# Performance work log

Measured on AMD Instinct MI355X. Metric: run time of the kernel, lower is better.

Reference implementation:

```python
import jax, jax.numpy as jnp
import numpy as np

E, IN, HID, OUT, B = 8, 512, 512, 512, 1024
BN_EPS = 1e-5

def _init_w(key, e, i, o):
    bound = np.sqrt(6.0 / (i * o))
    return jax.random.uniform(key, (e, i, o), dtype=jnp.float32, minval=-bound, maxval=bound)

def setup_inputs() -> dict:
    key = jax.random.key(0)
    k = jax.random.split(key, 6)
    x = jax.random.normal(k[0], (B, IN), dtype=jnp.float32)
    coef = jax.random.uniform(k[1], (B, E), dtype=jnp.float32)
    coef = coef / jnp.sum(coef, axis=-1, keepdims=True)  # soft blending weights
    w1 = _init_w(k[2], E, IN, HID)
    b1 = jnp.zeros((E, HID), dtype=jnp.float32)
    w2 = _init_w(k[3], E, HID, OUT)
    b2 = jnp.zeros((E, OUT), dtype=jnp.float32)
    gamma = jnp.ones((HID,), dtype=jnp.float32)
    beta = jnp.zeros((HID,), dtype=jnp.float32)
    return {"x": x, "blending_coef": coef, "w1": w1, "b1": b1,
            "w2": w2, "b2": b2, "gamma": gamma, "beta": beta}

def reference(x, blending_coef, w1, b1, w2, b2, gamma, beta):
    # layer 1: per-sample blended linear. Same math as
    # sum(coef[...,None,None]*w1, dim=1) applied via sum(x[...,None]*W, dim=1),
    # expressed as one contraction to avoid the [B,I,H] intermediate.
    h = jnp.einsum('be,eih,bi->bh', blending_coef, w1, x) + blending_coef @ b1
    # BatchNorm1d (training mode: batch stats, biased variance) + affine
    mean = jnp.mean(h, axis=0)
    var = jnp.mean((h - mean) ** 2, axis=0)
    hn = (h - mean) * jax.lax.rsqrt(var + BN_EPS) * gamma + beta
    h1 = jax.nn.elu(hn)
    # layer 2
    out = jnp.einsum('be,eho,bh->bo', blending_coef, w2, h1) + blending_coef @ b2
    return out
```

## Files before the change

kernel.cpp:

```cpp
#include <hip/hip_runtime.h>


typedef short bf16x8 __attribute__((ext_vector_type(8)));
typedef float f32x4 __attribute__((ext_vector_type(4)));
typedef unsigned short u16;
typedef u16 u16x4 __attribute__((ext_vector_type(4)));
typedef u16 u16x8 __attribute__((ext_vector_type(8)));

__device__ __forceinline__ u16 f2bf(float f) {
  union { float f; unsigned u; } v; v.f = f;
  return (u16)((v.u + 0x7FFFu + ((v.u >> 16) & 1u)) >> 16);
}
__device__ __forceinline__ float bf2f(u16 u) {
  union { unsigned u; float f; } v; v.u = (unsigned)u << 16; return v.f;
}

__global__ __launch_bounds__(256) void prep1_kernel(
    const float* __restrict__ x, const float* __restrict__ w1,
    u16* __restrict__ xbp, u16* __restrict__ w1p)
{
  int bid = blockIdx.x, t = threadIdx.x;
  __shared__ float ld[64][65];
  if (bid < 64) {
    int g = bid, ri = t & 15, q = t >> 4;
    #pragma unroll
    for (int rep = 0; rep < 4; ++rep) {
      int chunk = rep * 16 + q;
      int s = chunk >> 2, c = chunk & 3;
      const float* src = x + (size_t)(g * 16 + ri) * 512 + s * 32 + c * 8;
      f32x4 v0 = *(const f32x4*)src;
      f32x4 v1 = *(const f32x4*)(src + 4);
      u16x8 o;
      #pragma unroll
      for (int i = 0; i < 4; ++i) { o[i] = f2bf(v0[i]); o[4 + i] = f2bf(v1[i]); }
      *(u16x8*)(xbp + ((size_t)(g * 16 + s) * 64 + c * 16 + ri) * 8) = o;
    }
    return;
  }
  int job = bid - 64;
  int e = job >> 6, tl = job & 63;
  int kt = tl >> 3, nt = tl & 7;
  #pragma unroll
  for (int j = 0; j < 4; ++j) {
    int kr = j * 16 + (t >> 4), nc = (t & 15) * 4;
    f32x4 v = *(const f32x4*)(w1 + (size_t)(e * 512 + kt * 64 + kr) * 512 + nt * 64 + nc);
    ld[kr][nc] = v.x; ld[kr][nc + 1] = v.y; ld[kr][nc + 2] = v.z; ld[kr][nc + 3] = v.w;
  }
  __syncthreads();
  #pragma unroll
  for (int rep = 0; rep < 2; ++rep) {
    int gidx = rep * 256 + t;
    int ri = gidx & 15, c = (gidx >> 4) & 3, sl = (gidx >> 6) & 1, grp = gidx >> 7;
    int n_local = grp * 16 + ri;
    int gn = nt * 4 + grp, s = kt * 2 + sl, k0 = sl * 32 + c * 8;
    u16x8 o;
    #pragma unroll
    for (int i = 0; i < 8; ++i) o[i] = f2bf(ld[k0 + i][n_local]);
    *(u16x8*)(w1p + ((size_t)((e * 32 + gn) * 16 + s) * 64 + c * 16 + ri) * 8) = o;
  }
}

__global__ __launch_bounds__(512, 2) void gemm1_prep2(
    const u16* __restrict__ Ap, const u16* __restrict__ Wp,
    const float* __restrict__ coef, const float* __restrict__ bias,
    const float* __restrict__ w2, u16* __restrict__ w2p,
    u16* __restrict__ hb, float* __restrict__ sP, float* __restrict__ qP)
{
  __shared__ __align__(16) char smem[38912];
  int t = threadIdx.x;
  if (blockIdx.x >= 256) {
    float (*ld)[65] = (float (*)[65])smem;
    int job = blockIdx.x - 256;
    int e = job >> 6, tl = job & 63;
    int kt = tl >> 3, nt = tl & 7;
    #pragma unroll
    for (int j = 0; j < 2; ++j) {
      int kr = j * 32 + (t >> 4), nc = (t & 15) * 4;
      f32x4 v = *(const f32x4*)(w2 + (size_t)(e * 512 + kt * 64 + kr) * 512 + nt * 64 + nc);
      ld[kr][nc] = v.x; ld[kr][nc + 1] = v.y; ld[kr][nc + 2] = v.z; ld[kr][nc + 3] = v.w;
    }
    __syncthreads();
    {
      int ri = t & 15, c = (t >> 4) & 3, sl = (t >> 6) & 1, grp = t >> 7;
      int n_local = grp * 16 + ri;
      int gn = nt * 4 + grp, s = kt * 2 + sl, k0 = sl * 32 + c * 8;
      u16x8 o;
      #pragma unroll
      for (int i = 0; i < 8; ++i) o[i] = f2bf(ld[k0 + i][n_local]);
      *(u16x8*)(w2p + ((size_t)((e * 32 + gn) * 16 + s) * 64 + c * 16 + ri) * 8) = o;
    }
    return;
  }
  float* red = (float*)smem;
  f32x4* partS = (f32x4*)(smem + 34816);
  f32x4* partQ = (f32x4*)(smem + 34816 + 2048);
  int raw = blockIdx.x, nt = raw & 7, mt = raw >> 3;
  int l = t & 63, e = t >> 6;

  const u16* Ab = Ap + (size_t)(mt * 2) * 16 * 512 + l * 8;
  const u16* Bb = Wp + (size_t)(e * 32 + nt * 4) * 16 * 512 + l * 8;

  f32x4 acc[2][4] = {};
  bf16x8 bfr[3][4], afr[2][2];
  #pragma unroll
  for (int n = 0; n < 4; ++n) {
    bfr[0][n] = *(const bf16x8*)(Bb + (size_t)n * 16 * 512);
    bfr[1][n] = *(const bf16x8*)(Bb + (size_t)n * 16 * 512 + 512);
  }
  #pragma unroll
  for (int m = 0; m < 2; ++m)
    afr[0][m] = *(const bf16x8*)(Ab + (size_t)m * 16 * 512);

  #pragma unroll
  for (int s = 0; s < 16; ++s) {
    const int cb = s % 3, nb = (s + 2) % 3, ca = s & 1, na = ca ^ 1;
    if (s < 14) {
      #pragma unroll
      for (int n = 0; n < 4; ++n)
        bfr[nb][n] = *(const bf16x8*)(Bb + (size_t)n * 16 * 512 + (s + 2) * 512);
    }
    if (s < 15) {
      #pragma unroll
      for (int m = 0; m < 2; ++m)
        afr[na][m] = *(const bf16x8*)(Ab + (size_t)m * 16 * 512 + (s + 1) * 512);
    }
    #pragma unroll
    for (int m = 0; m < 2; ++m)
      #pragma unroll
      for (int n = 0; n < 4; ++n)
        acc[m][n] = __builtin_amdgcn_mfma_f32_16x16x32_bf16(afr[ca][m], bfr[cb][n], acc[m][n], 0, 0, 0);
  }

  int rl = (l >> 4) * 4;
  #pragma unroll
  for (int m = 0; m < 2; ++m)
    #pragma unroll
    for (int r = 0; r < 4; ++r) {
      float cf = coef[(size_t)(mt * 32 + m * 16 + rl + r) * 8 + e];
      #pragma unroll
      for (int n = 0; n < 4; ++n) acc[m][n][r] *= cf;
    }

#define RED_STORE(slot)                                                       \
  { _Pragma("unroll") for (int m = 0; m < 2; ++m)                             \
    _Pragma("unroll") for (int n = 0; n < 4; ++n)                             \
    _Pragma("unroll") for (int r = 0; r < 4; ++r)                             \
      red[(slot) * 2176 + (m * 16 + rl + r) * 68 + n * 16 + (l & 15)] = acc[m][n][r]; }
#define RED_ADD(slot)                                                         \
  { _Pragma("unroll") for (int m = 0; m < 2; ++m)                             \
    _Pragma("unroll") for (int n = 0; n < 4; ++n)                             \
    _Pragma("unroll") for (int r = 0; r < 4; ++r)                             \
      acc[m][n][r] += red[(slot) * 2176 + (m * 16 + rl + r) * 68 + n * 16 + (l & 15)]; }

  if (e >= 4) RED_STORE(e - 4);
  __syncthreads();
  if (e < 4) { RED_ADD(e); RED_STORE(e); }
  __syncthreads();

  {
    int row = t >> 4, c0 = (t & 15) * 4;
    f32x4 v = {0.f, 0.f, 0.f, 0.f};
    #pragma unroll
    for (int sl = 0; sl < 4; ++sl)
      v += *(const f32x4*)&red[sl * 2176 + row * 68 + c0];
    int rowg = mt * 32 + row, colg = nt * 64 + c0;
    f32x4 cv0 = *(const f32x4*)(coef + (size_t)rowg * 8);
    f32x4 cv1 = *(const f32x4*)(coef + (size_t)rowg * 8 + 4);
    #pragma unroll
    for (int e2 = 0; e2 < 4; ++e2) {
      v += cv0[e2] * *(const f32x4*)(bias + e2 * 512 + colg);
      v += cv1[e2] * *(const f32x4*)(bias + (e2 + 4) * 512 + colg);
    }
    f32x4 ss = v, qq = v * v;
    #pragma unroll
    for (int i = 0; i < 4; ++i) {
      ss[i] += __shfl_xor(ss[i], 16); ss[i] += __shfl_xor(ss[i], 32);
      qq[i] += __shfl_xor(qq[i], 16); qq[i] += __shfl_xor(qq[i], 32);
    }
    int w = t >> 6;
    if (l < 16) { partS[w * 16 + l] = ss; partQ[w * 16 + l] = qq; }
    u16x4 o;
    #pragma unroll
    for (int i = 0; i < 4; ++i) o[i] = f2bf(v[i]);
    int g = row >> 4, ri = row & 15;
    int spk = nt * 2 + (c0 >> 5), cpk = (c0 >> 3) & 3, j = c0 & 7;
    *(u16x4*)(hb + ((size_t)((mt * 2 + g) * 16 + spk) * 64 + cpk * 16 + ri) * 8 + j) = o;
  }
  __syncthreads();
  if (t < 16) {
    f32x4 S = {0.f, 0.f, 0.f, 0.f}, Q = {0.f, 0.f, 0.f, 0.f};
    #pragma unroll
    for (int w = 0; w < 8; ++w) { S += partS[w * 16 + t]; Q += partQ[w * 16 + t]; }
    *(f32x4*)(sP + mt * 512 + nt * 64 + t * 4) = S;
    *(f32x4*)(qP + mt * 512 + nt * 64 + t * 4) = Q;
  }
#undef RED_STORE
#undef RED_ADD
}

__global__ __launch_bounds__(512, 2) void gemm2_kernel(
    const u16* __restrict__ hb, const u16* __restrict__ Wp,
    const float* __restrict__ coef, const float* __restrict__ bias,
    const float* __restrict__ gamma, const float* __restrict__ beta,
    const float* __restrict__ sP, const float* __restrict__ qP,
    float* __restrict__ Out)
{
  __shared__ __align__(16) char smem[34816];
  __shared__ float sc[512], sh[512];
  u16* As = (u16*)smem;
  float* red = (float*)smem;
  int raw = blockIdx.x, nt = raw & 7, mt = raw >> 3;
  int t = threadIdx.x, l = t & 63, e = t >> 6;

  const u16* Bb = Wp + (size_t)(e * 32 + nt * 4) * 16 * 512 + l * 8;
  bf16x8 bfr[3][4];
  #pragma unroll
  for (int n = 0; n < 4; ++n) {
    bfr[0][n] = *(const bf16x8*)(Bb + (size_t)n * 16 * 512);
    bfr[1][n] = *(const bf16x8*)(Bb + (size_t)n * 16 * 512 + 512);
  }

  {
    float S = 0.f, Q = 0.f;
    #pragma unroll
    for (int p = 0; p < 32; ++p) { S += sP[p * 512 + t]; Q += qP[p * 512 + t]; }
    float mean = S * (1.0f / 1024.0f);
    float var  = Q * (1.0f / 1024.0f) - mean * mean;
    float s_ = gamma[t] * rsqrtf(var + 1e-5f);
    sc[t] = s_; sh[t] = beta[t] - mean * s_;
  }
  __syncthreads();

  const u16* hsrc = hb + (size_t)mt * 16384;
  #pragma unroll
  for (int rep = 0; rep < 4; ++rep) {
    int ci = rep * 512 + t;
    u16x8 hv = *(const u16x8*)(hsrc + (size_t)ci * 8);
    int s = (ci >> 6) & 15, c = (l >> 4) & 3;
    int k0 = s * 32 + c * 8;
    f32x4 s0 = *(const f32x4*)&sc[k0], s1 = *(const f32x4*)&sc[k0 + 4];
    f32x4 h0 = *(const f32x4*)&sh[k0], h1 = *(const f32x4*)&sh[k0 + 4];
    u16x8 o;
    #pragma unroll
    for (int i = 0; i < 4; ++i) {
      float v = bf2f(hv[i]) * s0[i] + h0[i];
      o[i] = f2bf(v > 0.f ? v : expm1f(v));
    }
    #pragma unroll
    for (int i = 0; i < 4; ++i) {
      float v = bf2f(hv[4 + i]) * s1[i] + h1[i];
      o[4 + i] = f2bf(v > 0.f ? v : expm1f(v));
    }
    *(u16x8*)&As[(size_t)ci * 8] = o;
  }
  __syncthreads();

  f32x4 acc[2][4] = {};
  #pragma unroll
  for (int s = 0; s < 16; ++s) {
    const int cb = s % 3, nb = (s + 2) % 3;
    if (s < 14) {
      #pragma unroll
      for (int n = 0; n < 4; ++n)
        bfr[nb][n] = *(const bf16x8*)(Bb + (size_t)n * 16 * 512 + (s + 2) * 512);
    }
    bf16x8 af[2];
    #pragma unroll
    for (int m = 0; m < 2; ++m)
      af[m] = *(const bf16x8*)&As[((m * 16 + s) * 64 + l) * 8];
    #pragma unroll
    for (int m = 0; m < 2; ++m)
      #pragma unroll
      for (int n = 0; n < 4; ++n)
        acc[m][n] = __builtin_amdgcn_mfma_f32_16x16x32_bf16(af[m], bfr[cb][n], acc[m][n], 0, 0, 0);
  }
  __syncthreads();

  int rl = (l >> 4) * 4;
  #pragma unroll
  for (int m = 0; m < 2; ++m)
    #pragma unroll
    for (int r = 0; r < 4; ++r) {
      float cf = coef[(size_t)(mt * 32 + m * 16 + rl + r) * 8 + e];
      #pragma unroll
      for (int n = 0; n < 4; ++n) acc[m][n][r] *= cf;
    }

#define RED_STORE(slot)                                                       \
  { _Pragma("unroll") for (int m = 0; m < 2; ++m)                             \
    _Pragma("unroll") for (int n = 0; n < 4; ++n)                             \
    _Pragma("unroll") for (int r = 0; r < 4; ++r)                             \
      red[(slot) * 2176 + (m * 16 + rl + r) * 68 + n * 16 + (l & 15)] = acc[m][n][r]; }
#define RED_ADD(slot)                                                         \
  { _Pragma("unroll") for (int m = 0; m < 2; ++m)                             \
    _Pragma("unroll") for (int n = 0; n < 4; ++n)                             \
    _Pragma("unroll") for (int r = 0; r < 4; ++r)                             \
      acc[m][n][r] += red[(slot) * 2176 + (m * 16 + rl + r) * 68 + n * 16 + (l & 15)]; }

  if (e >= 4) RED_STORE(e - 4);
  __syncthreads();
  if (e < 4) { RED_ADD(e); RED_STORE(e); }
  __syncthreads();

  {
    int row = t >> 4, c0 = (t & 15) * 4;
    f32x4 v = {0.f, 0.f, 0.f, 0.f};
    #pragma unroll
    for (int sl = 0; sl < 4; ++sl)
      v += *(const f32x4*)&red[sl * 2176 + row * 68 + c0];
    int rowg = mt * 32 + row, colg = nt * 64 + c0;
    f32x4 cv0 = *(const f32x4*)(coef + (size_t)rowg * 8);
    f32x4 cv1 = *(const f32x4*)(coef + (size_t)rowg * 8 + 4);
    #pragma unroll
    for (int e2 = 0; e2 < 4; ++e2) {
      v += cv0[e2] * *(const f32x4*)(bias + e2 * 512 + colg);
      v += cv1[e2] * *(const f32x4*)(bias + (e2 + 4) * 512 + colg);
    }
    *(f32x4*)(Out + (size_t)rowg * 512 + colg) = v;
  }
#undef RED_STORE
#undef RED_ADD
}

extern "C" void kernel_launch(void* const* d_in, const int* in_sizes, int n_in,
                              void* d_out, int out_size, void* d_ws, size_t ws_size,
                              hipStream_t stream)
{
  const float* x     = (const float*)d_in[0];
  const float* coef  = (const float*)d_in[1];
  const float* w1    = (const float*)d_in[2];
  const float* b1    = (const float*)d_in[3];
  const float* w2    = (const float*)d_in[4];
  const float* b2    = (const float*)d_in[5];
  const float* gamma = (const float*)d_in[6];
  const float* beta  = (const float*)d_in[7];
  float* out = (float*)d_out;

  char* ws = (char*)d_ws;
  u16* w1p  = (u16*)(ws);
  u16* w2p  = (u16*)(ws + (4u << 20));
  u16* xbp  = (u16*)(ws + (8u << 20));
  u16* hb   = (u16*)(ws + (9u << 20));
  float* sP = (float*)(ws + (10u << 20));
  float* qP = (float*)(ws + (10u << 20) + 65536);

  prep1_kernel<<<576, 256, 0, stream>>>(x, w1, xbp, w1p);
  gemm1_prep2<<<768, 512, 0, stream>>>(xbp, w1p, coef, b1, w2, w2p, hb, sP, qP);
  gemm2_kernel<<<256, 512, 0, stream>>>(hb, w2p, coef, b2, gamma, beta, sP, qP, out);
}
```

Before: 40.10 us.

## Move w2 conversion into prep kernel and shorten GEMM prefetch depth

The w2 fp32-to-bf16 repacking moves out of the GEMM1 launch and into the first prep kernel, so GEMM1 runs only its 256 compute blocks and no longer shares the GPU with conversion blocks. Both GEMMs drop from a three-deep to a two-deep register prefetch of B fragments. GEMM1 also stops double-buffering A fragments and loads them in the same step they are used. This lowers register pressure and simplifies scheduling, but it exposes more load latency in the MFMA loop and gives up the overlap of w2 conversion with GEMM1 compute.

```diff
diff --git a/kernel.cpp b/kernel.cpp
--- a/kernel.cpp
+++ b/kernel.cpp
@@ -15,9 +15,10 @@
   union { unsigned u; float f; } v; v.u = (unsigned)u << 16; return v.f;
 }
 
-__global__ __launch_bounds__(256) void prep1_kernel(
+__global__ __launch_bounds__(256) void prep_kernel(
     const float* __restrict__ x, const float* __restrict__ w1,
-    u16* __restrict__ xbp, u16* __restrict__ w1p)
+    const float* __restrict__ w2, u16* __restrict__ xbp,
+    u16* __restrict__ w1p, u16* __restrict__ w2p)
 {
   int bid = blockIdx.x, t = threadIdx.x;
   __shared__ float ld[64][65];
@@ -38,12 +39,14 @@
     return;
   }
   int job = bid - 64;
-  int e = job >> 6, tl = job & 63;
+  const float* src = (job >> 9) ? w2 : w1;
+  u16* dst = (job >> 9) ? w2p : w1p;
+  int rem = job & 511, e = rem >> 6, tl = rem & 63;
   int kt = tl >> 3, nt = tl & 7;
   #pragma unroll
   for (int j = 0; j < 4; ++j) {
     int kr = j * 16 + (t >> 4), nc = (t & 15) * 4;
-    f32x4 v = *(const f32x4*)(w1 + (size_t)(e * 512 + kt * 64 + kr) * 512 + nt * 64 + nc);
+    f32x4 v = *(const f32x4*)(src + (size_t)(e * 512 + kt * 64 + kr) * 512 + nt * 64 + nc);
     ld[kr][nc] = v.x; ld[kr][nc + 1] = v.y; ld[kr][nc + 2] = v.z; ld[kr][nc + 3] = v.w;
   }
   __syncthreads();
@@ -56,79 +59,48 @@
     u16x8 o;
     #pragma unroll
     for (int i = 0; i < 8; ++i) o[i] = f2bf(ld[k0 + i][n_local]);
-    *(u16x8*)(w1p + ((size_t)((e * 32 + gn) * 16 + s) * 64 + c * 16 + ri) * 8) = o;
-  }
-}
-
-__global__ __launch_bounds__(512, 2) void gemm1_prep2(
+    *(u16x8*)(dst + ((size_t)((e * 32 + gn) * 16 + s) * 64 + c * 16 + ri) * 8) = o;
+  }
+}
+
+__global__ __launch_bounds__(512, 2) void gemm1_kernel(
     const u16* __restrict__ Ap, const u16* __restrict__ Wp,
     const float* __restrict__ coef, const float* __restrict__ bias,
-    const float* __restrict__ w2, u16* __restrict__ w2p,
     u16* __restrict__ hb, float* __restrict__ sP, float* __restrict__ qP)
 {
   __shared__ __align__(16) char smem[38912];
-  int t = threadIdx.x;
-  if (blockIdx.x >= 256) {
-    float (*ld)[65] = (float (*)[65])smem;
-    int job = blockIdx.x - 256;
-    int e = job >> 6, tl = job & 63;
-    int kt = tl >> 3, nt = tl & 7;
-    #pragma unroll
-    for (int j = 0; j < 2; ++j) {
-      int kr = j * 32 + (t >> 4), nc = (t & 15) * 4;
-      f32x4 v = *(const f32x4*)(w2 + (size_t)(e * 512 + kt * 64 + kr) * 512 + nt * 64 + nc);
-      ld[kr][nc] = v.x; ld[kr][nc + 1] = v.y; ld[kr][nc + 2] = v.z; ld[kr][nc + 3] = v.w;
-    }
-    __syncthreads();
-    {
-      int ri = t & 15, c = (t >> 4) & 3, sl = (t >> 6) & 1, grp = t >> 7;
-      int n_local = grp * 16 + ri;
-      int gn = nt * 4 + grp, s = kt * 2 + sl, k0 = sl * 32 + c * 8;
-      u16x8 o;
-      #pragma unroll
-      for (int i = 0; i < 8; ++i) o[i] = f2bf(ld[k0 + i][n_local]);
-      *(u16x8*)(w2p + ((size_t)((e * 32 + gn) * 16 + s) * 64 + c * 16 + ri) * 8) = o;
-    }
-    return;
-  }
   float* red = (float*)smem;
   f32x4* partS = (f32x4*)(smem + 34816);
   f32x4* partQ = (f32x4*)(smem + 34816 + 2048);
   int raw = blockIdx.x, nt = raw & 7, mt = raw >> 3;
-  int l = t & 63, e = t >> 6;
+  int t = threadIdx.x, l = t & 63, e = t >> 6;
 
   const u16* Ab = Ap + (size_t)(mt * 2) * 16 * 512 + l * 8;
   const u16* Bb = Wp + (size_t)(e * 32 + nt * 4) * 16 * 512 + l * 8;
 
   f32x4 acc[2][4] = {};
-  bf16x8 bfr[3][4], afr[2][2];
-  #pragma unroll
-  for (int n = 0; n < 4; ++n) {
+  bf16x8 bfr[2][4];
+  #pragma unroll
+  for (int n = 0; n < 4; ++n)
     bfr[0][n] = *(const bf16x8*)(Bb + (size_t)n * 16 * 512);
-    bfr[1][n] = *(const bf16x8*)(Bb + (size_t)n * 16 * 512 + 512);
-  }
-  #pragma unroll
-  for (int m = 0; m < 2; ++m)
-    afr[0][m] = *(const bf16x8*)(Ab + (size_t)m * 16 * 512);
 
   #pragma unroll
   for (int s = 0; s < 16; ++s) {
-    const int cb = s % 3, nb = (s + 2) % 3, ca = s & 1, na = ca ^ 1;
-    if (s < 14) {
+    const int cur = s & 1, nxt = cur ^ 1;
+    if (s < 15) {
       #pragma unroll
       for (int n = 0; n < 4; ++n)
-        bfr[nb][n] = *(const bf16x8*)(Bb + (size_t)n * 16 * 512 + (s + 2) * 512);
-    }
-    if (s < 15) {
-      #pragma unroll
-      for (int m = 0; m < 2; ++m)
-        afr[na][m] = *(const bf16x8*)(Ab + (size_t)m * 16 * 512 + (s + 1) * 512);
-    }
+        bfr[nxt][n] = *(const bf16x8*)(Bb + (size_t)n * 16 * 512 + (s + 1) * 512);
+    }
+    bf16x8 af[2];
     #pragma unroll
     for (int m = 0; m < 2; ++m)
+      af[m] = *(const bf16x8*)(Ab + (size_t)m * 16 * 512 + s * 512);
+    #pragma unroll
+    for (int m = 0; m < 2; ++m)
       #pragma unroll
       for (int n = 0; n < 4; ++n)
-        acc[m][n] = __builtin_amdgcn_mfma_f32_16x16x32_bf16(afr[ca][m], bfr[cb][n], acc[m][n], 0, 0, 0);
+        acc[m][n] = __builtin_amdgcn_mfma_f32_16x16x32_bf16(af[m], bfr[cur][n], acc[m][n], 0, 0, 0);
   }
 
   int rl = (l >> 4) * 4;
@@ -213,12 +185,10 @@
   int t = threadIdx.x, l = t & 63, e = t >> 6;
 
   const u16* Bb = Wp + (size_t)(e * 32 + nt * 4) * 16 * 512 + l * 8;
-  bf16x8 bfr[3][4];
-  #pragma unroll
-  for (int n = 0; n < 4; ++n) {
+  bf16x8 bfr[2][4];
+  #pragma unroll
+  for (int n = 0; n < 4; ++n)
     bfr[0][n] = *(const bf16x8*)(Bb + (size_t)n * 16 * 512);
-    bfr[1][n] = *(const bf16x8*)(Bb + (size_t)n * 16 * 512 + 512);
-  }
 
   {
     float S = 0.f, Q = 0.f;
@@ -258,11 +228,11 @@
   f32x4 acc[2][4] = {};
   #pragma unroll
   for (int s = 0; s < 16; ++s) {
-    const int cb = s % 3, nb = (s + 2) % 3;
-    if (s < 14) {
+    const int cur = s & 1, nxt = cur ^ 1;
+    if (s < 15) {
       #pragma unroll
       for (int n = 0; n < 4; ++n)
-        bfr[nb][n] = *(const bf16x8*)(Bb + (size_t)n * 16 * 512 + (s + 2) * 512);
+        bfr[nxt][n] = *(const bf16x8*)(Bb + (size_t)n * 16 * 512 + (s + 1) * 512);
     }
     bf16x8 af[2];
     #pragma unroll
@@ -272,7 +242,7 @@
     for (int m = 0; m < 2; ++m)
       #pragma unroll
       for (int n = 0; n < 4; ++n)
-        acc[m][n] = __builtin_amdgcn_mfma_f32_16x16x32_bf16(af[m], bfr[cb][n], acc[m][n], 0, 0, 0);
+        acc[m][n] = __builtin_amdgcn_mfma_f32_16x16x32_bf16(af[m], bfr[cur][n], acc[m][n], 0, 0, 0);
   }
   __syncthreads();
 
@@ -344,7 +314,7 @@
   float* sP = (float*)(ws + (10u << 20));
   float* qP = (float*)(ws + (10u << 20) + 65536);
 
-  prep1_kernel<<<576, 256, 0, stream>>>(x, w1, xbp, w1p);
-  gemm1_prep2<<<768, 512, 0, stream>>>(xbp, w1p, coef, b1, w2, w2p, hb, sP, qP);
+  prep_kernel<<<1088, 256, 0, stream>>>(x, w1, w2, xbp, w1p, w2p);
+  gemm1_kernel<<<256, 512, 0, stream>>>(xbp, w1p, coef, b1, hb, sP, qP);
   gemm2_kernel<<<256, 512, 0, stream>>>(hb, w2p, coef, b2, gamma, beta, sP, qP, out);
 }
```

Result: faster. 38.32 us (-4.4%).
